# Optimization experiments

Hardware: AMD Instinct MI355X
Metric: run time of the kernel (lower is better)

## Reference

```python
import jax, jax.numpy as jnp
import numpy as np

B, P, D = 8, 1024, 768
H = 12
HD = D // H


def setup_inputs() -> dict:
    key = jax.random.key(0)
    k1, k2, k3, k4, k5 = jax.random.split(key, 5)
    s = 0.02
    return {
        "x": jax.random.normal(k1, (B, P, D), dtype=jnp.float32),
        "w_qkv": jax.random.normal(k2, (D, 3 * D), dtype=jnp.float32) * s,
        "b_qkv": jax.random.normal(k3, (3 * D,), dtype=jnp.float32) * s,
        "w_proj": jax.random.normal(k4, (D, D), dtype=jnp.float32) * s,
        "b_proj": jax.random.normal(k5, (D,), dtype=jnp.float32) * s,
    }


def reference(x, w_qkv, b_qkv, w_proj, b_proj):
    b, p, d = x.shape
    scale = HD ** -0.5
    qkv = x @ w_qkv + b_qkv                      # [B,P,3D]
    qkv = qkv.reshape(b, p, 3, H, HD).transpose(2, 0, 3, 1, 4)  # [3,B,H,P,HD]
    q, k, v = qkv[0], qkv[1], qkv[2]
    attn = jnp.einsum("bhqd,bhkd->bhqk", q, k) * scale
    attn = jax.nn.softmax(attn, axis=-1)         # attn_drop is identity (p=0)
    weighted_avg = jnp.einsum("bhqk,bhkd->bhqd", attn, v)
    weighted_avg = weighted_avg.transpose(0, 2, 1, 3).reshape(b, p, d)  # [B,P,D]
    out = weighted_avg @ w_proj + b_proj         # proj_drop is identity (p=0)
    return (out, weighted_avg)
```

## Files before the change

### kernel.cpp

```cpp
#include <hip/hip_runtime.h>
#include <hip/hip_bf16.h>


typedef __attribute__((ext_vector_type(8))) short short8;
typedef __attribute__((ext_vector_type(4))) float f32x4;

#define MFMA_BF16(a, b, c) __builtin_amdgcn_mfma_f32_16x16x32_bf16((a), (b), (c), 0, 0, 0)

#define NB 8
#define NP 1024
#define ND 768
#define NH 12
#define NHD 64
#define NTOK (NB * NP)
#define N3D (3 * ND)
#define OUT_HALF (NTOK * ND)
#define QSCALE 0.18033688f

__device__ __forceinline__ void gload_lds16(const void* gptr, void* ldsptr) {
  __builtin_amdgcn_global_load_lds(
      (const __attribute__((address_space(1))) unsigned int*)gptr,
      (__attribute__((address_space(3))) unsigned int*)ldsptr, 16, 0, 0);
}

__device__ __forceinline__ unsigned pack_bf16x2(float a, float b) {
  __hip_bfloat162 h = __float22bfloat162_rn(float2{a, b});
  return *reinterpret_cast<unsigned*>(&h);
}

__device__ __forceinline__ int swz_g(int b) { return b ^ (((b >> 7) & 7) << 4); }


__global__ void k_cvt_x(const float* __restrict__ in, __hip_bfloat16* __restrict__ out) {
  int i = (blockIdx.x * 256 + threadIdx.x) * 8;
  float4 a = *(const float4*)(in + i);
  float4 b = *(const float4*)(in + i + 4);
  union { __hip_bfloat16 h[8]; uint4 u; } r;
  r.h[0] = __float2bfloat16(a.x); r.h[1] = __float2bfloat16(a.y);
  r.h[2] = __float2bfloat16(a.z); r.h[3] = __float2bfloat16(a.w);
  r.h[4] = __float2bfloat16(b.x); r.h[5] = __float2bfloat16(b.y);
  r.h[6] = __float2bfloat16(b.z); r.h[7] = __float2bfloat16(b.w);
  *(uint4*)(out + i) = r.u;
}

__global__ void k_cvt_t(const float* __restrict__ in, __hip_bfloat16* __restrict__ out,
                        int K, int N) {
  __shared__ float tile[32][33];
  int k0 = blockIdx.x * 32;
  int n0 = blockIdx.y * 32;
  int r = threadIdx.x >> 5;
  int c = threadIdx.x & 31;
#pragma unroll
  for (int i = 0; i < 4; ++i)
    tile[r + 8 * i][c] = in[(size_t)(k0 + r + 8 * i) * N + n0 + c];
  __syncthreads();
#pragma unroll
  for (int i = 0; i < 4; ++i)
    out[(size_t)(n0 + r + 8 * i) * K + k0 + c] = __float2bfloat16(tile[c][r + 8 * i]);
}


__device__ __forceinline__ void gemm_mainloop(const __hip_bfloat16* __restrict__ A,
                                              const __hip_bfloat16* __restrict__ BT,
                                              int m0, int n0, char* Ls,
                                              f32x4 acc[4][4]) {
  const int tid = threadIdx.x;
  const int wid = tid >> 6, lane = tid & 63;
  const int wm = wid >> 1, wn = wid & 1;
  const int lrow = lane & 15, lk = lane >> 4;
  constexpr int K = 768, NKT = K / 32;

  int aoff[4], boff[4];
#pragma unroll
  for (int i = 0; i < 4; ++i) {
    aoff[i] = swz_g((wm * 64 + i * 16 + lrow) * 64 + lk * 16);
    boff[i] = swz_g((wn * 64 + i * 16 + lrow) * 64 + lk * 16);
  }

#define STAGE_G(kt, bi)                                                  \
  {                                                                      \
    const int k0s = (kt) * 32;                                           \
    char* dst = Ls + (bi) * 16384;                                       \
    _Pragma("unroll")                                                    \
    for (int t = 0; t < 2; ++t) {                                        \
      const int L = (tid + t * 256) * 16;          \
      const int lb = swz_g(L);              \
      const int mr = lb >> 6;                   \
      const int kk = (lb & 63) >> 1;            \
      gload_lds16(A + (size_t)(m0 + mr) * K + k0s + kk,                  \
                  dst + wid * 1024 + t * 4096);                          \
      gload_lds16(BT + (size_t)(n0 + mr) * K + k0s + kk,                 \
                  dst + 8192 + wid * 1024 + t * 4096);                   \
    }                                                                    \
  }

#define COMPUTE_T(kt)                                                          \
  {                                                                            \
    const char* buf = Ls + ((kt) % 3) * 16384;                                 \
    short8 af[4], bf[4];                                                       \
    _Pragma("unroll")                                                          \
    for (int i = 0; i < 4; ++i) {                                              \
      af[i] = *(const short8*)(buf + aoff[i]);                                 \
      bf[i] = *(const short8*)(buf + 8192 + boff[i]);                          \
    }                                                                          \
    _Pragma("unroll")                                                          \
    for (int mi = 0; mi < 4; ++mi)                                             \
      _Pragma("unroll")                                                        \
      for (int ni = 0; ni < 4; ++ni)                                           \
        acc[mi][ni] = MFMA_BF16(af[mi], bf[ni], acc[mi][ni]);                  \
  }

  STAGE_G(0, 0);
  STAGE_G(1, 1);

#pragma unroll 3
  for (int kt = 0; kt < NKT - 1; ++kt) {
    asm volatile("s_waitcnt vmcnt(4)" ::: "memory");
    __builtin_amdgcn_s_barrier();
    if (kt + 2 < NKT) STAGE_G(kt + 2, (kt + 2) % 3);
    COMPUTE_T(kt);
  }
  asm volatile("s_waitcnt vmcnt(0)" ::: "memory");
  __builtin_amdgcn_s_barrier();
  COMPUTE_T(NKT - 1);

#undef STAGE_G
#undef COMPUTE_T
}


__launch_bounds__(256)
__global__ void k_qkv_gemm(const __hip_bfloat16* __restrict__ A,
                           const __hip_bfloat16* __restrict__ BT,
                           const float* __restrict__ bias,
                           __hip_bfloat16* __restrict__ q_ws,
                           __hip_bfloat16* __restrict__ k_ws,
                           __hip_bfloat16* __restrict__ v_ws) {
  __shared__ char Ls[3 * 16384];
  const int mt = blockIdx.x & 63, nt = blockIdx.x >> 6;
  const int m0 = mt * 128, n0 = nt * 128;
  const int wid = threadIdx.x >> 6, lane = threadIdx.x & 63;
  const int wm = wid >> 1, wn = wid & 1;
  const int lrow = lane & 15, lk = lane >> 4;

  f32x4 acc[4][4] = {};
  gemm_mainloop(A, BT, m0, n0, Ls, acc);

  const int which = n0 / ND;
#pragma unroll
  for (int ni = 0; ni < 4; ++ni) {
    const int n = n0 + wn * 64 + ni * 16 + lrow;
    const float bv = bias[n];
    const int hh = (n % ND) >> 6;
    const int hd = n & 63;
#pragma unroll
    for (int mi = 0; mi < 4; ++mi) {
      const int mbase = m0 + wm * 64 + mi * 16 + lk * 4;
#pragma unroll
      for (int i = 0; i < 4; ++i) {
        const int m = mbase + i;
        const float v = acc[mi][ni][i] + bv;
        const int b = m >> 10, p = m & 1023;
        const int bh = b * NH + hh;
        if (which == 0)      q_ws[((size_t)bh * NP + p) * NHD + hd] = __float2bfloat16(v * QSCALE);
        else if (which == 1) k_ws[((size_t)bh * NP + p) * NHD + hd] = __float2bfloat16(v);
        else                 v_ws[((size_t)bh * NHD + hd) * NP + p] = __float2bfloat16(v);
      }
    }
  }
}


#define KVBLK 64

__launch_bounds__(256)
__global__ void k_attn(const __hip_bfloat16* __restrict__ q_ws,
                       const __hip_bfloat16* __restrict__ k_ws,
                       const __hip_bfloat16* __restrict__ v_ws,
                       float* __restrict__ wavg_f32,
                       __hip_bfloat16* __restrict__ wavg_bf) {
  __shared__ char smem[2 * 16384 + 4 * 4608];
  const int bid = blockIdx.x;
  const int wg = (bid & 7) * 96 + (bid >> 3);
  const int bh = wg >> 3, qb = wg & 7;
  const int tid = threadIdx.x;
  const int wid = tid >> 6, lane = tid & 63;
  const int lrow = lane & 15, lk = lane >> 4;
  const int q0 = qb * 128 + wid * 32;
  char* pbuf = smem + 32768 + wid * 4608;

  const __hip_bfloat16* Qb = q_ws + (size_t)bh * NP * NHD;
  const __hip_bfloat16* Kb = k_ws + (size_t)bh * NP * NHD;
  const __hip_bfloat16* Vb = v_ws + (size_t)bh * NHD * NP;

  short8 qf[2][2];
#pragma unroll
  for (int g = 0; g < 2; ++g) {
    qf[g][0] = *(const short8*)(Qb + (size_t)(q0 + g * 16 + lrow) * NHD + lk * 8);
    qf[g][1] = *(const short8*)(Qb + (size_t)(q0 + g * 16 + lrow) * NHD + 32 + lk * 8);
  }

  f32x4 acc[2][4] = {};
  float dsum[2] = {0.f, 0.f};

#define STAGE(buf, key0)                                                          \
  {                                                                               \
    _Pragma("unroll")                                                             \
    for (int p = 0; p < 2; ++p) {                                                 \
      const int L = p * 4096 + tid * 16;                                          \
      const int r = L >> 7;                                                       \
      const int cb = L & 127;                                                     \
      const int sc = (cb ^ ((r & 7) << 4)) >> 1;        \
      gload_lds16(Kb + (size_t)((key0) + r) * NHD + sc, (buf) + L);               \
      gload_lds16(Vb + (size_t)r * NP + (key0) + sc, (buf) + 8192 + L);           \
    }                                                                             \
  }

  char* cur = smem;
  char* nxt = smem + 16384;
  STAGE(cur, 0);
  __syncthreads();

  for (int kc = 0; kc < NP / KVBLK; ++kc) {
    if (kc < NP / KVBLK - 1) STAGE(nxt, (kc + 1) * KVBLK);

    char* Ks = cur;
    char* Vs = cur + 8192;

    f32x4 s[2][4];
    __builtin_amdgcn_s_setprio(1);
#pragma unroll
    for (int kt = 0; kt < 4; ++kt) {
      const int row = kt * 16 + lrow;
      const int sw = (row & 7) << 4;
      short8 klo = *(const short8*)(Ks + row * 128 + ((lk * 16) ^ sw));
      short8 khi = *(const short8*)(Ks + row * 128 + ((64 + lk * 16) ^ sw));
      f32x4 z = {0.f, 0.f, 0.f, 0.f};
      s[0][kt] = MFMA_BF16(klo, qf[0][0], z);
      s[0][kt] = MFMA_BF16(khi, qf[0][1], s[0][kt]);
      s[1][kt] = MFMA_BF16(klo, qf[1][0], z);
      s[1][kt] = MFMA_BF16(khi, qf[1][1], s[1][kt]);
    }
    __builtin_amdgcn_s_setprio(0);

#pragma unroll
    for (int g = 0; g < 2; ++g)
#pragma unroll
      for (int kt = 0; kt < 4; ++kt) {
        const float p0 = __builtin_amdgcn_exp2f(s[g][kt][0]);
        const float p1 = __builtin_amdgcn_exp2f(s[g][kt][1]);
        const float p2 = __builtin_amdgcn_exp2f(s[g][kt][2]);
        const float p3 = __builtin_amdgcn_exp2f(s[g][kt][3]);
        dsum[g] += (p0 + p1) + (p2 + p3);
        uint2 w;
        w.x = pack_bf16x2(p0, p1);
        w.y = pack_bf16x2(p2, p3);
        *(uint2*)(pbuf + (g * 16 + lrow) * 144 + kt * 32 + lk * 8) = w;
      }

    __builtin_amdgcn_s_setprio(1);
#pragma unroll
    for (int kh = 0; kh < 2; ++kh) {
      short8 a20 = *(const short8*)(pbuf + lrow * 144 + kh * 64 + lk * 16);
      short8 a21 = *(const short8*)(pbuf + (16 + lrow) * 144 + kh * 64 + lk * 16);
#pragma unroll
      for (int hdt = 0; hdt < 4; ++hdt) {
        const int row = hdt * 16 + lrow;
        short8 vf = *(const short8*)(Vs + row * 128 +
                                     ((kh * 64 + lk * 16) ^ ((row & 7) << 4)));
        acc[0][hdt] = MFMA_BF16(a20, vf, acc[0][hdt]);
        acc[1][hdt] = MFMA_BF16(a21, vf, acc[1][hdt]);
      }
    }
    __builtin_amdgcn_s_setprio(0);

    __syncthreads();
    char* t = cur; cur = nxt; nxt = t;
  }

  const int b = bh / NH, hh = bh % NH;
#pragma unroll
  for (int g = 0; g < 2; ++g) {
    float ds = dsum[g];
    ds += __shfl_xor(ds, 16);
    ds += __shfl_xor(ds, 32);
    float rd[4];
#pragma unroll
    for (int i = 0; i < 4; ++i) rd[i] = 1.0f / __shfl(ds, lk * 4 + i, 16);

#pragma unroll
    for (int hdt = 0; hdt < 4; ++hdt) {
#pragma unroll
      for (int i = 0; i < 4; ++i) {
        const int qq = q0 + g * 16 + lk * 4 + i;
        const int col = hh * NHD + hdt * 16 + lrow;
        const float val = acc[g][hdt][i] * rd[i];
        const size_t o = ((size_t)b * NP + qq) * ND + col;
        wavg_f32[o] = val;
        wavg_bf[o] = __float2bfloat16(val);
      }
    }
  }
#undef STAGE
}


__launch_bounds__(256)
__global__ void k_proj_gemm(const __hip_bfloat16* __restrict__ A,
                            const __hip_bfloat16* __restrict__ BT,
                            const float* __restrict__ bias,
                            float* __restrict__ C) {
  __shared__ char Ls[3 * 16384];
  const int mt = blockIdx.x & 63, nt = blockIdx.x >> 6;
  const int m0 = mt * 128, n0 = nt * 128;
  const int wid = threadIdx.x >> 6, lane = threadIdx.x & 63;
  const int wm = wid >> 1, wn = wid & 1;
  const int lrow = lane & 15, lk = lane >> 4;

  f32x4 acc[4][4] = {};
  gemm_mainloop(A, BT, m0, n0, Ls, acc);

#pragma unroll
  for (int ni = 0; ni < 4; ++ni) {
    const int n = n0 + wn * 64 + ni * 16 + lrow;
    const float bv = bias[n];
#pragma unroll
    for (int mi = 0; mi < 4; ++mi) {
      const int mbase = m0 + wm * 64 + mi * 16 + lk * 4;
#pragma unroll
      for (int i = 0; i < 4; ++i)
        C[(size_t)(mbase + i) * ND + n] = acc[mi][ni][i] + bv;
    }
  }
}


extern "C" void kernel_launch(void* const* d_in, const int* in_sizes, int n_in,
                              void* d_out, int out_size, void* d_ws, size_t ws_size,
                              hipStream_t stream) {
  const float* x      = (const float*)d_in[0];
  const float* w_qkv  = (const float*)d_in[1];
  const float* b_qkv  = (const float*)d_in[2];
  const float* w_proj = (const float*)d_in[3];
  const float* b_proj = (const float*)d_in[4];
  float* out = (float*)d_out;
  float* wavg_out = out + OUT_HALF;

  char* ws = (char*)d_ws;
  __hip_bfloat16* xbf    = (__hip_bfloat16*)(ws);
  __hip_bfloat16* wqkvT  = (__hip_bfloat16*)(ws + 12582912);
  __hip_bfloat16* wprojT = (__hip_bfloat16*)(ws + 16121856);
  __hip_bfloat16* q_ws   = (__hip_bfloat16*)(ws + 17301504);
  __hip_bfloat16* k_ws   = (__hip_bfloat16*)(ws + 29884416);
  __hip_bfloat16* v_ws   = (__hip_bfloat16*)(ws + 42467328);
  __hip_bfloat16* wavg_bf = xbf;

  k_cvt_x<<<NTOK * ND / (256 * 8), 256, 0, stream>>>(x, xbf);
  k_cvt_t<<<dim3(ND / 32, N3D / 32), 256, 0, stream>>>(w_qkv, wqkvT, ND, N3D);
  k_cvt_t<<<dim3(ND / 32, ND / 32), 256, 0, stream>>>(w_proj, wprojT, ND, ND);
  k_qkv_gemm<<<(NTOK / 128) * (N3D / 128), 256, 0, stream>>>(xbf, wqkvT, b_qkv,
                                                             q_ws, k_ws, v_ws);
  k_attn<<<(NP / 128) * (NB * NH), 256, 0, stream>>>(q_ws, k_ws, v_ws, wavg_out, wavg_bf);
  k_proj_gemm<<<(NTOK / 128) * (ND / 128), 256, 0, stream>>>(wavg_bf, wprojT, b_proj, out);
}
```

Baseline: 130.7 us.

## Switch GEMM mainloop from triple to double LDS buffering with register prefetch

The shared GEMM mainloop in the QKV and projection kernels now uses two 16 KB LDS stages instead of three, cutting static LDS per block from 48 KB to 32 KB. Each iteration loads its A/B fragments into registers, waits on LDS reads, and barriers. It then issues the async global-to-LDS load for tile kt+2 into the buffer just consumed, before running the MFMAs. The aim is to fit more resident blocks per CU, at the cost of a second barrier per k-step and a shallower prefetch distance.

Result: no change. 131.3 us (+0.4%).

```diff
diff --git a/kernel.cpp b/kernel.cpp
--- a/kernel.cpp
+++ b/kernel.cpp
@@ -94,38 +94,51 @@
     }                                                                    \
   }
 
-#define COMPUTE_T(kt)                                                          \
-  {                                                                            \
-    const char* buf = Ls + ((kt) % 3) * 16384;                                 \
-    short8 af[4], bf[4];                                                       \
-    _Pragma("unroll")                                                          \
-    for (int i = 0; i < 4; ++i) {                                              \
-      af[i] = *(const short8*)(buf + aoff[i]);                                 \
-      bf[i] = *(const short8*)(buf + 8192 + boff[i]);                          \
-    }                                                                          \
-    _Pragma("unroll")                                                          \
-    for (int mi = 0; mi < 4; ++mi)                                             \
-      _Pragma("unroll")                                                        \
-      for (int ni = 0; ni < 4; ++ni)                                           \
-        acc[mi][ni] = MFMA_BF16(af[mi], bf[ni], acc[mi][ni]);                  \
-  }
-
   STAGE_G(0, 0);
   STAGE_G(1, 1);
 
-#pragma unroll 3
+#pragma unroll 2
   for (int kt = 0; kt < NKT - 1; ++kt) {
     asm volatile("s_waitcnt vmcnt(4)" ::: "memory");
     __builtin_amdgcn_s_barrier();
-    if (kt + 2 < NKT) STAGE_G(kt + 2, (kt + 2) % 3);
-    COMPUTE_T(kt);
-  }
+
+    const char* buf = Ls + (kt & 1) * 16384;
+    short8 af[4], bf[4];
+#pragma unroll
+    for (int i = 0; i < 4; ++i) {
+      af[i] = *(const short8*)(buf + aoff[i]);
+      bf[i] = *(const short8*)(buf + 8192 + boff[i]);
+    }
+
+    asm volatile("s_waitcnt lgkmcnt(0)" ::: "memory");
+    __builtin_amdgcn_s_barrier();
+
+    if (kt + 2 < NKT) STAGE_G(kt + 2, kt & 1);
+
+#pragma unroll
+    for (int mi = 0; mi < 4; ++mi)
+#pragma unroll
+      for (int ni = 0; ni < 4; ++ni)
+        acc[mi][ni] = MFMA_BF16(af[mi], bf[ni], acc[mi][ni]);
+  }
+
   asm volatile("s_waitcnt vmcnt(0)" ::: "memory");
   __builtin_amdgcn_s_barrier();
-  COMPUTE_T(NKT - 1);
-
+  {
+    const char* buf = Ls + ((NKT - 1) & 1) * 16384;
+    short8 af[4], bf[4];
+#pragma unroll
+    for (int i = 0; i < 4; ++i) {
+      af[i] = *(const short8*)(buf + aoff[i]);
+      bf[i] = *(const short8*)(buf + 8192 + boff[i]);
+    }
+#pragma unroll
+    for (int mi = 0; mi < 4; ++mi)
+#pragma unroll
+      for (int ni = 0; ni < 4; ++ni)
+        acc[mi][ni] = MFMA_BF16(af[mi], bf[ni], acc[mi][ni]);
+  }
 #undef STAGE_G
-#undef COMPUTE_T
 }
 
 
@@ -136,7 +149,7 @@
                            __hip_bfloat16* __restrict__ q_ws,
                            __hip_bfloat16* __restrict__ k_ws,
                            __hip_bfloat16* __restrict__ v_ws) {
-  __shared__ char Ls[3 * 16384];
+  __shared__ char Ls[2 * 16384];
   const int mt = blockIdx.x & 63, nt = blockIdx.x >> 6;
   const int m0 = mt * 128, n0 = nt * 128;
   const int wid = threadIdx.x >> 6, lane = threadIdx.x & 63;
@@ -310,7 +323,7 @@
                             const __hip_bfloat16* __restrict__ BT,
                             const float* __restrict__ bias,
                             float* __restrict__ C) {
-  __shared__ char Ls[3 * 16384];
+  __shared__ char Ls[2 * 16384];
   const int mt = blockIdx.x & 63, nt = blockIdx.x >> 6;
   const int m0 = mt * 128, n0 = nt * 128;
   const int wid = threadIdx.x >> 6, lane = threadIdx.x & 63;
```
